# Kernel optimization log

Measured on AMD Instinct MI355X. Metric: run time of the kernel, lower is better.

## Reference

```python
import jax, jax.numpy as jnp
import numpy as np

B, S, D, H, DK = 2, 2048, 1024, 16, 64
NUM_BUCKETS, MAX_DIST = 32, 128
EPS = 1e-6


def _relative_position_bucket(rel, num_buckets=NUM_BUCKETS, max_distance=MAX_DIST):
    # bidirectional (T5 encoder) bucketing
    nb = num_buckets // 2
    bucket = (rel > 0).astype(jnp.int32) * nb
    n = jnp.abs(rel)
    max_exact = nb // 2
    is_small = n < max_exact
    large = max_exact + (
        jnp.log(jnp.maximum(n, 1).astype(jnp.float32) / max_exact)
        / np.log(max_distance / max_exact)
        * (nb - max_exact)
    ).astype(jnp.int32)
    large = jnp.minimum(large, nb - 1)
    return bucket + jnp.where(is_small, n, large)


def softmax1(logits):
    # off-by-one softmax: exp(x-m) / (sum(exp(x-m)) + exp(-m))
    m = jax.lax.stop_gradient(jnp.max(logits, axis=-1, keepdims=True))
    e = jnp.exp(logits - m)
    return e / (jnp.sum(e, axis=-1, keepdims=True) + jnp.exp(-m))


def setup_inputs() -> dict:
    key = jax.random.key(0)
    ks = jax.random.split(key, 8)
    scale = 0.02
    return {
        "hidden_states": jax.random.normal(ks[0], (B, S, D), dtype=jnp.float32),
        "delete_gate_mask": jax.random.normal(ks[1], (B, S, 1), dtype=jnp.float32),
        "ln_w": jnp.ones((D,), dtype=jnp.float32),
        "q_w": jax.random.normal(ks[2], (D, H * DK), dtype=jnp.float32) * scale,
        "k_w": jax.random.normal(ks[3], (D, H * DK), dtype=jnp.float32) * scale,
        "v_w": jax.random.normal(ks[4], (D, H * DK), dtype=jnp.float32) * scale,
        "o_w": jax.random.normal(ks[5], (H * DK, D), dtype=jnp.float32) * scale,
        "rel_emb": jax.random.normal(ks[6], (NUM_BUCKETS, H), dtype=jnp.float32) * scale,
    }


def reference(hidden_states, delete_gate_mask, ln_w, q_w, k_w, v_w, o_w, rel_emb):
    # T5LayerNorm (RMS norm, no mean subtraction, no bias)
    var = jnp.mean(jnp.square(hidden_states), axis=-1, keepdims=True)
    x = hidden_states * jax.lax.rsqrt(var + EPS) * ln_w

    # projections (T5 Linear layers have no bias, no 1/sqrt(d) scaling)
    q = (x @ q_w).reshape(B, S, H, DK).transpose(0, 2, 1, 3)  # bhqd
    k = (x @ k_w).reshape(B, S, H, DK).transpose(0, 2, 1, 3)  # bhkd
    v = (x @ v_w).reshape(B, S, H, DK).transpose(0, 2, 1, 3)  # bhkd

    scores = jnp.einsum("bhqd,bhkd->bhqk", q, k)

    # relative position bias: [1, H, S, S]
    pos = jnp.arange(S)
    rel = pos[None, :] - pos[:, None]  # key_pos - query_pos
    bucket = _relative_position_bucket(rel)  # [S, S]
    position_bias = rel_emb[bucket].transpose(2, 0, 1)[None]  # [1,H,S,S]

    # delete gate: [B,S,1] -> additive mask over key axis [B,1,1,S]
    gate = delete_gate_mask[..., 0][:, None, None, :]

    scores = scores + position_bias + gate
    attn = softmax1(scores.astype(jnp.float32)).astype(scores.dtype)

    attn_out = jnp.einsum("bhqk,bhkd->bhqd", attn, v)
    attn_out = attn_out.transpose(0, 2, 1, 3).reshape(B, S, H * DK) @ o_w

    # residual (dropout disabled at p=0)
    return hidden_states + attn_out
```

## Files before the change

### kernel.cpp

```cpp
#include <hip/hip_runtime.h>
#include <hip/hip_bf16.h>
#include <math.h>

typedef __attribute__((ext_vector_type(8))) short short8;
typedef __attribute__((ext_vector_type(4))) float f32x4;

#define S_LEN   2048
#define DMODEL  1024
#define NHEAD   16
#define HDK     64
#define NBATCH  2
#define MTOT    (NBATCH*S_LEN)
#define LOG2E   1.4426950408889634f

__device__ __forceinline__ unsigned short f2bf(float f) {
  union { float f; unsigned u; } c; c.f = f;
  unsigned r = c.u + 0x7FFFu + ((c.u >> 16) & 1u);
  return (unsigned short)(r >> 16);
}
__device__ __forceinline__ float bf2f(unsigned short u) {
  union { unsigned u; float f; } c; c.u = ((unsigned)u) << 16;
  return c.f;
}

__device__ __forceinline__ short8 lds_ld16(const unsigned short* p) {
  return *reinterpret_cast<const short8*>(p);
}

__device__ __forceinline__ void gload_lds16(const unsigned short* g, unsigned short* l) {
  __builtin_amdgcn_global_load_lds(
      (const __attribute__((address_space(1))) unsigned int*)g,
      (__attribute__((address_space(3))) unsigned int*)l, 16, 0, 0);
}

__global__ __launch_bounds__(256) void transpose_w_kernel(
    const float* __restrict__ qw, const float* __restrict__ kw,
    const float* __restrict__ vw, const float* __restrict__ ow,
    unsigned short* __restrict__ wqkv, unsigned short* __restrict__ wo) {
  int z = blockIdx.z;
  const float* src = (z==0)?qw:(z==1)?kw:(z==2)?vw:ow;
  unsigned short* dst = (z<3) ? (wqkv + (size_t)z*DMODEL*DMODEL) : wo;
  __shared__ float tile[32][33];
  int n0 = blockIdx.x*32, k0 = blockIdx.y*32;
  int tx = threadIdx.x, ty = threadIdx.y;
  for (int r = ty; r < 32; r += 8)
    tile[r][tx] = src[(size_t)(k0+r)*DMODEL + n0 + tx];
  __syncthreads();
  for (int r = ty; r < 32; r += 8)
    dst[(size_t)(n0+r)*DMODEL + k0 + tx] = f2bf(tile[tx][r]);
}

__global__ void bias_table_kernel(const float* __restrict__ rel_emb,
                                  float* __restrict__ btab) {
  int idx = blockIdx.x*256 + threadIdx.x;
  if (idx >= NHEAD*4095) return;
  int h = idx / 4095, rp = idx % 4095, rel = rp - 2047;
  int bucket = (rel > 0) ? 16 : 0;
  int n = (rel < 0) ? -rel : rel;
  int v;
  if (n < 8) v = n;
  else {
    float lrv = logf((float)n * 0.125f) / 2.7725887f * 8.0f;
    v = 8 + (int)lrv;
    if (v > 15) v = 15;
  }
  btab[idx] = rel_emb[(size_t)(bucket + v)*NHEAD + h] * LOG2E;
}

__global__ void eg_kernel(const float* __restrict__ gmask,
                          float* __restrict__ egf,
                          unsigned short* __restrict__ egb) {
  int i = blockIdx.x*256 + threadIdx.x;
  float e = __expf(gmask[i]);
  egf[i] = e;
  egb[i] = f2bf(e);
}

__global__ __launch_bounds__(256) void rmsnorm_kernel(
    const float* __restrict__ hs, const float* __restrict__ lnw,
    unsigned short* __restrict__ xo) {
  int row = blockIdx.x, t = threadIdx.x;
  const float4 v = ((const float4*)(hs + (size_t)row*DMODEL))[t];
  float ss = v.x*v.x + v.y*v.y + v.z*v.z + v.w*v.w;
  #pragma unroll
  for (int off = 32; off >= 1; off >>= 1) ss += __shfl_xor(ss, off, 64);
  __shared__ float wsum[4];
  if ((t & 63) == 0) wsum[t >> 6] = ss;
  __syncthreads();
  float tot = wsum[0] + wsum[1] + wsum[2] + wsum[3];
  float sc = rsqrtf(tot * (1.0f/DMODEL) + 1e-6f);
  const float4 lw = ((const float4*)lnw)[t];
  uint2 o;
  o.x = (unsigned)f2bf(v.x*sc*lw.x) | ((unsigned)f2bf(v.y*sc*lw.y) << 16);
  o.y = (unsigned)f2bf(v.z*sc*lw.z) | ((unsigned)f2bf(v.w*sc*lw.w) << 16);
  ((uint2*)(xo + (size_t)row*DMODEL))[t] = o;
}

template<int EPI>
__global__ __launch_bounds__(256) void gemm128(
    const unsigned short* __restrict__ X,
    const unsigned short* __restrict__ W,
    unsigned short* __restrict__ Oq, unsigned short* __restrict__ Ok,
    unsigned short* __restrict__ Ov,
    const float* __restrict__ resid, float* __restrict__ Of,
    const float* __restrict__ escale) {
  __shared__ unsigned short As[128*64];
  __shared__ unsigned short Bs[128*64];
  const int z = blockIdx.z;
  int m0, n0;
  const unsigned short *Ap, *Bp;
  if (EPI == 0 && z == 2) {
    m0 = blockIdx.y*128; n0 = blockIdx.x*128;
    Ap = W + (size_t)2*DMODEL*DMODEL; Bp = X;
  } else {
    m0 = blockIdx.x*128; n0 = blockIdx.y*128;
    Ap = X; Bp = W + ((EPI==0) ? (size_t)z*DMODEL*DMODEL : 0);
  }
  const int t = threadIdx.x, lane = t & 63, w = t >> 6;
  const int g = lane >> 4, lr = lane & 15;
  const int wr = (w >> 1)*64, wc = (w & 1)*64;

  f32x4 acc[4][4];
  #pragma unroll
  for (int mi = 0; mi < 4; mi++)
    #pragma unroll
    for (int ni = 0; ni < 4; ni++) acc[mi][ni] = (f32x4){0.f,0.f,0.f,0.f};

  const unsigned short* ag[4]; const unsigned short* bg[4];
  unsigned short* al[4]; unsigned short* bl[4];
  #pragma unroll
  for (int i = 0; i < 4; i++) {
    int slot = t + i*256, row = slot >> 3, c8 = slot & 7;
    int cs = c8 ^ (row & 7);
    ag[i] = Ap + (size_t)(m0 + row)*DMODEL + cs*8;
    bg[i] = Bp + (size_t)(n0 + row)*DMODEL + cs*8;
    al[i] = As + slot*8;
    bl[i] = Bs + slot*8;
  }

  for (int kk = 0; kk < DMODEL; kk += 64) {
    #pragma unroll
    for (int i = 0; i < 4; i++) {
      gload_lds16(ag[i] + kk, al[i]);
      gload_lds16(bg[i] + kk, bl[i]);
    }
    __syncthreads();
    #pragma unroll
    for (int ks = 0; ks < 2; ks++) {
      short8 af[4], bfr[4];
      #pragma unroll
      for (int mi = 0; mi < 4; mi++) {
        int R = wr + mi*16 + lr;
        af[mi] = lds_ld16(As + R*64 + (((ks*4 + g) ^ (R & 7)) << 3));
      }
      #pragma unroll
      for (int ni = 0; ni < 4; ni++) {
        int R = wc + ni*16 + lr;
        bfr[ni] = lds_ld16(Bs + R*64 + (((ks*4 + g) ^ (R & 7)) << 3));
      }
      #pragma unroll
      for (int mi = 0; mi < 4; mi++)
        #pragma unroll
        for (int ni = 0; ni < 4; ni++)
          acc[mi][ni] = __builtin_amdgcn_mfma_f32_16x16x32_bf16(af[mi], bfr[ni], acc[mi][ni], 0, 0, 0);
    }
    __syncthreads();
  }

  if (EPI == 0) {
    if (z < 2) {
      unsigned short* dst = (z == 0) ? Oq : Ok;
      const float osc = (z == 0) ? LOG2E : 1.0f;
      #pragma unroll
      for (int mi = 0; mi < 4; mi++) {
        #pragma unroll
        for (int r = 0; r < 4; r++) {
          int m = m0 + wr + mi*16 + g*4 + r;
          int b = m >> 11, s = m & (S_LEN-1);
          unsigned short* drow = dst + ((size_t)b*NHEAD*S_LEN + s)*HDK;
          #pragma unroll
          for (int ni = 0; ni < 4; ni++) {
            int n = n0 + wc + ni*16 + lr;
            int h = n >> 6, dcol = n & 63;
            drow[(size_t)h*S_LEN*HDK + dcol] = f2bf(acc[mi][ni][r] * osc);
          }
        }
      }
    } else {
      #pragma unroll
      for (int ni = 0; ni < 4; ni++) {
        int n = n0 + wc + ni*16 + lr;
        int b = n >> 11, s = n & (S_LEN-1);
        float e = escale[n];
        #pragma unroll
        for (int mi = 0; mi < 4; mi++)
          #pragma unroll
          for (int r = 0; r < 4; r++) {
            int m = m0 + wr + mi*16 + g*4 + r;
            Ov[((size_t)b*DMODEL + m)*S_LEN + s] = f2bf(acc[mi][ni][r] * e);
          }
      }
    }
  } else {
    #pragma unroll
    for (int mi = 0; mi < 4; mi++) {
      #pragma unroll
      for (int r = 0; r < 4; r++) {
        int m = m0 + wr + mi*16 + g*4 + r;
        const float* rrow = resid + (size_t)m*DMODEL;
        float* orow = Of + (size_t)m*DMODEL;
        #pragma unroll
        for (int ni = 0; ni < 4; ni++) {
          int n = n0 + wc + ni*16 + lr;
          orow[n] = rrow[n] + acc[mi][ni][r];
        }
      }
    }
  }
}

__global__ __launch_bounds__(256, 2) void combine_guard_dummy() {}
template<int SPLIT>
__global__ __launch_bounds__(256, 2) void attn_kernel(
    const unsigned short* __restrict__ Qg,
    const unsigned short* __restrict__ Kg,
    const unsigned short* __restrict__ Vtg,
    const float* __restrict__ btab,
    const unsigned short* __restrict__ egb,
    unsigned short* __restrict__ Og,
    unsigned short* __restrict__ Op0,
    unsigned short* __restrict__ Op1,
    float* __restrict__ lpart) {
  __shared__ __align__(16) unsigned short Kl[2][64][64];
  __shared__ __align__(16) unsigned short Vl[2][64][64];
  __shared__ __align__(16) unsigned short Pl[4][2][16*64];

  const int flat = blockIdx.x;
  const int xcd = flat & 7, j = flat >> 3;
  int bh, qx, half;
  if (SPLIT) { bh = xcd*4 + (j >> 5); int rest = j & 31; qx = rest >> 1; half = rest & 1; }
  else       { bh = xcd*4 + (j >> 4); qx = j & 15; half = 0; }
  const int b = bh >> 4, h = bh & 15;
  const int q0 = qx * 128;
  const int ktbase = SPLIT ? half*16 : 0;
  const int ktend  = SPLIT ? ktbase + 16 : 32;

  const int t = threadIdx.x, w = t >> 6, lane = t & 63;
  const int g = lane >> 4, lr = lane & 15, l7 = lane & 7;

  const unsigned short* Qb = Qg  + (size_t)bh*S_LEN*HDK;
  const unsigned short* Kb = Kg  + (size_t)bh*S_LEN*HDK;
  const unsigned short* Vb = Vtg + (size_t)bh*HDK*S_LEN;
  const unsigned short* ge = egb + (size_t)b*S_LEN;

  const int srow = t >> 3, sg0 = t & 7;
  const int cs = sg0 ^ (srow & 7);
  const unsigned short* kS0 = Kb + (size_t)srow*HDK + cs*8;
  const unsigned short* kS1 = Kb + (size_t)(srow+32)*HDK + cs*8;
  const unsigned short* vS0 = Vb + (size_t)srow*S_LEN + cs*8;
  const unsigned short* vS1 = Vb + (size_t)(srow+32)*S_LEN + cs*8;

#define STAGE(nb_, key_) do {                                          \
    gload_lds16(kS0 + (size_t)(key_)*HDK, &Kl[nb_][0][0] + t*8);       \
    gload_lds16(kS1 + (size_t)(key_)*HDK, &Kl[nb_][0][0] + t*8 + 2048);\
    gload_lds16(vS0 + (key_),             &Vl[nb_][0][0] + t*8);       \
    gload_lds16(vS1 + (key_),             &Vl[nb_][0][0] + t*8 + 2048);\
  } while (0)

  const int qs0A = q0 + w*32, qs0B = qs0A + 16;
  short8 qfA0 = *reinterpret_cast<const short8*>(Qb + (size_t)(qs0A+lr)*HDK + g*8);
  short8 qfA1 = *reinterpret_cast<const short8*>(Qb + (size_t)(qs0A+lr)*HDK + 32 + g*8);
  short8 qfB0 = *reinterpret_cast<const short8*>(Qb + (size_t)(qs0B+lr)*HDK + g*8);
  short8 qfB1 = *reinterpret_cast<const short8*>(Qb + (size_t)(qs0B+lr)*HDK + 32 + g*8);

  f32x4 accA[4], accB[4], l4A, l4B;
  #pragma unroll
  for (int n = 0; n < 4; n++) { accA[n] = (f32x4){0.f,0.f,0.f,0.f}; accB[n] = (f32x4){0.f,0.f,0.f,0.f}; }
  l4A = (f32x4){0.f,0.f,0.f,0.f}; l4B = (f32x4){0.f,0.f,0.f,0.f};

  const float* btb = btab + (size_t)h*4095 + 2047;
  const float cpos = btb[91];
  const float cneg = btb[-91];

  char* prowA = (char*)&Pl[w][0][0] + lr*128;
  char* prowB = (char*)&Pl[w][1][0] + lr*128;

  STAGE(0, ktbase*64);
  int cur = 0;
  for (int kt = ktbase; kt < ktend; ++kt) {
    const int key0 = kt*64;
    __syncthreads();

    if (kt + 1 < ktend) STAGE(cur^1, key0+64);

    short8 gv[2];
    #pragma unroll
    for (int c = 0; c < 2; c++) {
      short8 z8 = (short8){0,0,0,0,0,0,0,0};
      if (lr == 0)
        z8 = *reinterpret_cast<const short8*>(ge + key0 + c*32 + g*8);
      gv[c] = z8;
    }

    const int dbA = key0 - qs0A, dbB = key0 - qs0B;
    const bool bandA = (dbA > -154 && dbA < 106);
    const bool bandB = (dbB > -154 && dbB < 106);
    const float ccA = bandA ? 0.f : ((dbA > 0) ? cpos : cneg);
    const float ccB = bandB ? 0.f : ((dbB > 0) ? cpos : cneg);
    f32x4 svA[4], svB[4];
    {
      f32x4 zA = (f32x4){ccA,ccA,ccA,ccA}, zB = (f32x4){ccB,ccB,ccB,ccB};
      short8 bk[4];
      #pragma unroll
      for (int n = 0; n < 4; n++)
        bk[n] = lds_ld16(&Kl[cur][n*16 + lr][(g ^ l7) << 3]);
      __builtin_amdgcn_s_setprio(1);
      #pragma unroll
      for (int n = 0; n < 4; n++) {
        svA[n] = __builtin_amdgcn_mfma_f32_16x16x32_bf16(bk[n], qfA0, zA, 0, 0, 0);
        svB[n] = __builtin_amdgcn_mfma_f32_16x16x32_bf16(bk[n], qfB0, zB, 0, 0, 0);
      }
      __builtin_amdgcn_s_setprio(0);
      #pragma unroll
      for (int n = 0; n < 4; n++)
        bk[n] = lds_ld16(&Kl[cur][n*16 + lr][((4 + g) ^ l7) << 3]);
      __builtin_amdgcn_s_setprio(1);
      #pragma unroll
      for (int n = 0; n < 4; n++) {
        svA[n] = __builtin_amdgcn_mfma_f32_16x16x32_bf16(bk[n], qfA1, svA[n], 0, 0, 0);
        svB[n] = __builtin_amdgcn_mfma_f32_16x16x32_bf16(bk[n], qfB1, svB[n], 0, 0, 0);
      }
      __builtin_amdgcn_s_setprio(0);
    }

#define FINISH_SM(sv_, band_, db_, prow_)                                             \
    {                                                                                 \
      if (band_) {                                                                    \
        const float* btq = btb + ((db_) - lr);                                        \
        _Pragma("unroll") for (int n = 0; n < 4; n++)                                 \
          _Pragma("unroll") for (int r = 0; r < 4; r++)                               \
            sv_[n][r] += btq[n*16 + g*4 + r];                                         \
      }                                                                               \
      _Pragma("unroll") for (int n = 0; n < 4; n++)                                   \
        _Pragma("unroll") for (int r = 0; r < 4; r++)                                 \
          sv_[n][r] = exp2f(sv_[n][r]);                                               \
      _Pragma("unroll") for (int n = 0; n < 4; n++) {                                 \
        unsigned plo_, phi_;                                                          \
        asm("v_cvt_pk_bf16_f32 %0, %1, %2" : "=v"(plo_) : "v"(sv_[n][0]), "v"(sv_[n][1])); \
        asm("v_cvt_pk_bf16_f32 %0, %1, %2" : "=v"(phi_) : "v"(sv_[n][2]), "v"(sv_[n][3])); \
        uint2 pw_; pw_.x = plo_; pw_.y = phi_;                                        \
        *reinterpret_cast<uint2*>((prow_) + ((((2*n + (g>>1)) ^ l7) << 4) + ((g & 1) << 3))) = pw_; \
      }                                                                               \
    }
    FINISH_SM(svA, bandA, dbA, prowA)
    FINISH_SM(svB, bandB, dbB, prowB)
#undef FINISH_SM

    #pragma unroll
    for (int c = 0; c < 2; c++) {
      short8 bvf[4];
      #pragma unroll
      for (int n = 0; n < 4; n++)
        bvf[n] = lds_ld16(&Vl[cur][n*16 + lr][((4*c + g) ^ l7) << 3]);
      short8 paA = lds_ld16((const unsigned short*)(prowA + (((4*c + g) ^ l7) << 4)));
      short8 paB = lds_ld16((const unsigned short*)(prowB + (((4*c + g) ^ l7) << 4)));
      __builtin_amdgcn_s_setprio(1);
      #pragma unroll
      for (int n = 0; n < 4; n++) {
        accA[n] = __builtin_amdgcn_mfma_f32_16x16x32_bf16(paA, bvf[n], accA[n], 0, 0, 0);
        accB[n] = __builtin_amdgcn_mfma_f32_16x16x32_bf16(paB, bvf[n], accB[n], 0, 0, 0);
      }
      l4A = __builtin_amdgcn_mfma_f32_16x16x32_bf16(paA, gv[c], l4A, 0, 0, 0);
      l4B = __builtin_amdgcn_mfma_f32_16x16x32_bf16(paB, gv[c], l4B, 0, 0, 0);
      __builtin_amdgcn_s_setprio(0);
    }

    cur ^= 1;
  }

#define FINAL_SET(acc_, l4_, qs0_, op_)                                               \
  {                                                                                   \
    if (SPLIT) {                                                                      \
      if (lr == 0) {                                                                  \
        _Pragma("unroll") for (int r = 0; r < 4; r++)                                 \
          lpart[(size_t)half*(32*S_LEN) + (size_t)bh*S_LEN + (qs0_) + g*4 + r] = l4_[r]; \
      }                                                                               \
      _Pragma("unroll") for (int r = 0; r < 4; r++) {                                 \
        int srw = (qs0_) + g*4 + r;                                                   \
        unsigned short* orow = (op_) + ((size_t)bh*S_LEN + srw)*HDK;                  \
        _Pragma("unroll") for (int n = 0; n < 4; n++)                                 \
          orow[n*16 + lr] = f2bf(acc_[n][r]);                                         \
      }                                                                               \
    } else {                                                                          \
      _Pragma("unroll") for (int r = 0; r < 4; r++) {                                 \
        float lq = __shfl(l4_[r], g*16);                                              \
        float inv = 1.0f / (lq + 1.0f);                                               \
        int srw = (qs0_) + g*4 + r;                                                   \
        unsigned short* orow = Og + ((size_t)b*S_LEN + srw)*DMODEL + h*HDK;           \
        _Pragma("unroll") for (int n = 0; n < 4; n++)                                 \
          orow[n*16 + lr] = f2bf(acc_[n][r] * inv);                                   \
      }                                                                               \
    }                                                                                 \
  }
  unsigned short* op = half ? Op1 : Op0;
  FINAL_SET(accA, l4A, qs0A, op)
  FINAL_SET(accB, l4B, qs0B, op)
#undef FINAL_SET
#undef STAGE
}

__global__ __launch_bounds__(256) void combine_kernel(
    const unsigned short* __restrict__ Op0,
    const unsigned short* __restrict__ Op1,
    const float* __restrict__ lpart,
    unsigned short* __restrict__ ao) {
  int idx = blockIdx.x*256 + threadIdx.x;
  int row = idx >> 3;
  int d0 = (idx & 7) * 8;
  float l = lpart[row] + lpart[(size_t)32*S_LEN + row] + 1.0f;
  float inv = 1.0f / l;
  size_t src = (size_t)row*HDK + d0;
  short8 o0 = *reinterpret_cast<const short8*>(Op0 + src);
  short8 o1 = *reinterpret_cast<const short8*>(Op1 + src);
  int bh = row >> 11, s = row & (S_LEN-1), b = bh >> 4, h = bh & 15;
  unsigned short out[8];
  #pragma unroll
  for (int k = 0; k < 8; k++)
    out[k] = f2bf((bf2f((unsigned short)o0[k]) + bf2f((unsigned short)o1[k])) * inv);
  *reinterpret_cast<uint4*>(ao + ((size_t)(b*S_LEN + s))*DMODEL + h*HDK + d0) =
      *reinterpret_cast<const uint4*>(out);
}

extern "C" void kernel_launch(void* const* d_in, const int* in_sizes, int n_in,
                              void* d_out, int out_size, void* d_ws, size_t ws_size,
                              hipStream_t stream) {
  const float* hs   = (const float*)d_in[0];
  const float* gate = (const float*)d_in[1];
  const float* lnw  = (const float*)d_in[2];
  const float* qw   = (const float*)d_in[3];
  const float* kw   = (const float*)d_in[4];
  const float* vw   = (const float*)d_in[5];
  const float* ow   = (const float*)d_in[6];
  const float* rel  = (const float*)d_in[7];
  float* out = (float*)d_out;

  char* ws = (char*)d_ws;
  const size_t MB = 1ull << 20;
  unsigned short* xbf  = (unsigned short*)(ws);
  unsigned short* wqkv = (unsigned short*)(ws + 8*MB);
  unsigned short* wo   = (unsigned short*)(ws + 14*MB);
  unsigned short* qb   = (unsigned short*)(ws + 16*MB);
  unsigned short* kb   = (unsigned short*)(ws + 24*MB);
  unsigned short* vt   = (unsigned short*)(ws + 32*MB);
  unsigned short* ao   = (unsigned short*)(ws + 40*MB);
  float*          btab = (float*)(ws + 48*MB);
  float*          lpart= (float*)(ws + 48*MB + 256*1024);
  float*          egf  = (float*)(ws + 48*MB + 768*1024);
  unsigned short* egb  = (unsigned short*)(ws + 48*MB + 784*1024);
  unsigned short* op1  = (unsigned short*)(ws + 49*MB);
  unsigned short* op0  = xbf;
  const bool do_split = ws_size >= (57*MB);

  transpose_w_kernel<<<dim3(32,32,4), dim3(32,8), 0, stream>>>(qw, kw, vw, ow, wqkv, wo);
  bias_table_kernel<<<dim3(256), dim3(256), 0, stream>>>(rel, btab);
  eg_kernel<<<dim3(16), dim3(256), 0, stream>>>(gate, egf, egb);
  rmsnorm_kernel<<<dim3(MTOT), dim3(256), 0, stream>>>(hs, lnw, xbf);
  gemm128<0><<<dim3(MTOT/128, DMODEL/128, 3), dim3(256), 0, stream>>>(
      xbf, wqkv, qb, kb, vt, nullptr, nullptr, egf);
  if (do_split) {
    attn_kernel<1><<<dim3(1024), dim3(256), 0, stream>>>(
        qb, kb, vt, btab, egb, nullptr, op0, op1, lpart);
    combine_kernel<<<dim3(2048), dim3(256), 0, stream>>>(op0, op1, lpart, ao);
  } else {
    attn_kernel<0><<<dim3(512), dim3(256), 0, stream>>>(
        qb, kb, vt, btab, egb, ao, nullptr, nullptr, nullptr);
  }
  gemm128<1><<<dim3(MTOT/128, DMODEL/128, 1), dim3(256), 0, stream>>>(
      ao, wo, nullptr, nullptr, nullptr, hs, out, nullptr);
}
```

Measured before the change: 142.7 us.

## Drop split-K attention with combine; use 128-key tiles per barrier

Removes the two-way key-split attention path and its combine kernel, so each block processes all 2048 keys for its 128 queries with 512 blocks. K/V staging tiles grow from 64 to 128 keys, processed as two 64-key halves per barrier, which halves the number of synchronizations and deepens prefetch. This eliminates the partial-output write/read and an extra launch, at the cost of fewer blocks (less parallelism on many CUs) and doubled LDS use, which may reduce occupancy.

```diff
diff --git a/kernel.cpp b/kernel.cpp
--- a/kernel.cpp
+++ b/kernel.cpp
@@ -17,10 +17,6 @@
   union { float f; unsigned u; } c; c.f = f;
   unsigned r = c.u + 0x7FFFu + ((c.u >> 16) & 1u);
   return (unsigned short)(r >> 16);
-}
-__device__ __forceinline__ float bf2f(unsigned short u) {
-  union { unsigned u; float f; } c; c.u = ((unsigned)u) << 16;
-  return c.f;
 }
 
 __device__ __forceinline__ short8 lds_ld16(const unsigned short* p) {
@@ -219,31 +215,22 @@
   }
 }
 
-__global__ __launch_bounds__(256, 2) void combine_guard_dummy() {}
-template<int SPLIT>
 __global__ __launch_bounds__(256, 2) void attn_kernel(
     const unsigned short* __restrict__ Qg,
     const unsigned short* __restrict__ Kg,
     const unsigned short* __restrict__ Vtg,
     const float* __restrict__ btab,
     const unsigned short* __restrict__ egb,
-    unsigned short* __restrict__ Og,
-    unsigned short* __restrict__ Op0,
-    unsigned short* __restrict__ Op1,
-    float* __restrict__ lpart) {
-  __shared__ __align__(16) unsigned short Kl[2][64][64];
-  __shared__ __align__(16) unsigned short Vl[2][64][64];
+    unsigned short* __restrict__ Og) {
+  __shared__ __align__(16) unsigned short Kl[2][128*64];
+  __shared__ __align__(16) unsigned short Vl[2][64*128];
   __shared__ __align__(16) unsigned short Pl[4][2][16*64];
 
   const int flat = blockIdx.x;
   const int xcd = flat & 7, j = flat >> 3;
-  int bh, qx, half;
-  if (SPLIT) { bh = xcd*4 + (j >> 5); int rest = j & 31; qx = rest >> 1; half = rest & 1; }
-  else       { bh = xcd*4 + (j >> 4); qx = j & 15; half = 0; }
+  const int bh = xcd*4 + (j >> 4), qx = j & 15;
   const int b = bh >> 4, h = bh & 15;
   const int q0 = qx * 128;
-  const int ktbase = SPLIT ? half*16 : 0;
-  const int ktend  = SPLIT ? ktbase + 16 : 32;
 
   const int t = threadIdx.x, w = t >> 6, lane = t & 63;
   const int g = lane >> 4, lr = lane & 15, l7 = lane & 7;
@@ -253,19 +240,21 @@
   const unsigned short* Vb = Vtg + (size_t)bh*HDK*S_LEN;
   const unsigned short* ge = egb + (size_t)b*S_LEN;
 
-  const int srow = t >> 3, sg0 = t & 7;
-  const int cs = sg0 ^ (srow & 7);
-  const unsigned short* kS0 = Kb + (size_t)srow*HDK + cs*8;
-  const unsigned short* kS1 = Kb + (size_t)(srow+32)*HDK + cs*8;
-  const unsigned short* vS0 = Vb + (size_t)srow*S_LEN + cs*8;
-  const unsigned short* vS1 = Vb + (size_t)(srow+32)*S_LEN + cs*8;
-
+  const unsigned short* kS[4]; const unsigned short* vS[4]; int so[4];
+  #pragma unroll
+  for (int i = 0; i < 4; i++) {
+    int slot = t + i*256; so[i] = slot*8;
+    int krow = slot >> 3, kg = slot & 7;
+    kS[i] = Kb + (size_t)krow*HDK + ((kg ^ (krow & 7)) << 3);
+    int vrow = slot >> 4, vg = slot & 15;
+    int vcs = (vg & 8) | ((vg & 7) ^ (vrow & 7));
+    vS[i] = Vb + (size_t)vrow*S_LEN + vcs*8;
+  }
 #define STAGE(nb_, key_) do {                                          \
-    gload_lds16(kS0 + (size_t)(key_)*HDK, &Kl[nb_][0][0] + t*8);       \
-    gload_lds16(kS1 + (size_t)(key_)*HDK, &Kl[nb_][0][0] + t*8 + 2048);\
-    gload_lds16(vS0 + (key_),             &Vl[nb_][0][0] + t*8);       \
-    gload_lds16(vS1 + (key_),             &Vl[nb_][0][0] + t*8 + 2048);\
-  } while (0)
+    _Pragma("unroll") for (int i = 0; i < 4; i++) {                    \
+      gload_lds16(kS[i] + (size_t)(key_)*HDK, &Kl[nb_][0] + so[i]);    \
+      gload_lds16(vS[i] + (key_),             &Vl[nb_][0] + so[i]);    \
+    } } while (0)
 
   const int qs0A = q0 + w*32, qs0B = qs0A + 16;
   short8 qfA0 = *reinterpret_cast<const short8*>(Qb + (size_t)(qs0A+lr)*HDK + g*8);
@@ -285,150 +274,122 @@
   char* prowA = (char*)&Pl[w][0][0] + lr*128;
   char* prowB = (char*)&Pl[w][1][0] + lr*128;
 
-  STAGE(0, ktbase*64);
+  STAGE(0, 0);
   int cur = 0;
-  for (int kt = ktbase; kt < ktend; ++kt) {
-    const int key0 = kt*64;
+  for (int kt = 0; kt < S_LEN/128; ++kt) {
+    const int key0 = kt*128;
     __syncthreads();
 
-    if (kt + 1 < ktend) STAGE(cur^1, key0+64);
-
-    short8 gv[2];
+    if (kt + 1 < S_LEN/128) STAGE(cur^1, key0+128);
+
     #pragma unroll
-    for (int c = 0; c < 2; c++) {
-      short8 z8 = (short8){0,0,0,0,0,0,0,0};
-      if (lr == 0)
-        z8 = *reinterpret_cast<const short8*>(ge + key0 + c*32 + g*8);
-      gv[c] = z8;
-    }
-
-    const int dbA = key0 - qs0A, dbB = key0 - qs0B;
-    const bool bandA = (dbA > -154 && dbA < 106);
-    const bool bandB = (dbB > -154 && dbB < 106);
-    const float ccA = bandA ? 0.f : ((dbA > 0) ? cpos : cneg);
-    const float ccB = bandB ? 0.f : ((dbB > 0) ? cpos : cneg);
-    f32x4 svA[4], svB[4];
-    {
-      f32x4 zA = (f32x4){ccA,ccA,ccA,ccA}, zB = (f32x4){ccB,ccB,ccB,ccB};
-      short8 bk[4];
-      #pragma unroll
-      for (int n = 0; n < 4; n++)
-        bk[n] = lds_ld16(&Kl[cur][n*16 + lr][(g ^ l7) << 3]);
-      __builtin_amdgcn_s_setprio(1);
-      #pragma unroll
-      for (int n = 0; n < 4; n++) {
-        svA[n] = __builtin_amdgcn_mfma_f32_16x16x32_bf16(bk[n], qfA0, zA, 0, 0, 0);
-        svB[n] = __builtin_amdgcn_mfma_f32_16x16x32_bf16(bk[n], qfB0, zB, 0, 0, 0);
-      }
-      __builtin_amdgcn_s_setprio(0);
-      #pragma unroll
-      for (int n = 0; n < 4; n++)
-        bk[n] = lds_ld16(&Kl[cur][n*16 + lr][((4 + g) ^ l7) << 3]);
-      __builtin_amdgcn_s_setprio(1);
-      #pragma unroll
-      for (int n = 0; n < 4; n++) {
-        svA[n] = __builtin_amdgcn_mfma_f32_16x16x32_bf16(bk[n], qfA1, svA[n], 0, 0, 0);
-        svB[n] = __builtin_amdgcn_mfma_f32_16x16x32_bf16(bk[n], qfB1, svB[n], 0, 0, 0);
-      }
-      __builtin_amdgcn_s_setprio(0);
-    }
+    for (int hh = 0; hh < 2; hh++) {
+      const int k64 = key0 + hh*64;
+      const unsigned short* Klh = &Kl[cur][0] + hh*64*64;
+
+      short8 gvh[2];
+      #pragma unroll
+      for (int c = 0; c < 2; c++) {
+        short8 z8 = (short8){0,0,0,0,0,0,0,0};
+        if (lr == 0)
+          z8 = *reinterpret_cast<const short8*>(ge + k64 + c*32 + g*8);
+        gvh[c] = z8;
+      }
+
+      const int dbA = k64 - qs0A, dbB = k64 - qs0B;
+      const bool bandA = (dbA > -154 && dbA < 106);
+      const bool bandB = (dbB > -154 && dbB < 106);
+      const float ccA = bandA ? 0.f : ((dbA > 0) ? cpos : cneg);
+      const float ccB = bandB ? 0.f : ((dbB > 0) ? cpos : cneg);
+      f32x4 svA[4], svB[4];
+      {
+        f32x4 zA = (f32x4){ccA,ccA,ccA,ccA}, zB = (f32x4){ccB,ccB,ccB,ccB};
+        short8 bk[4];
+        #pragma unroll
+        for (int n = 0; n < 4; n++)
+          bk[n] = lds_ld16(Klh + (n*16 + lr)*64 + ((g ^ l7) << 3));
+        __builtin_amdgcn_s_setprio(1);
+        #pragma unroll
+        for (int n = 0; n < 4; n++) {
+          svA[n] = __builtin_amdgcn_mfma_f32_16x16x32_bf16(bk[n], qfA0, zA, 0, 0, 0);
+          svB[n] = __builtin_amdgcn_mfma_f32_16x16x32_bf16(bk[n], qfB0, zB, 0, 0, 0);
+        }
+        __builtin_amdgcn_s_setprio(0);
+        #pragma unroll
+        for (int n = 0; n < 4; n++)
+          bk[n] = lds_ld16(Klh + (n*16 + lr)*64 + (((4 + g) ^ l7) << 3));
+        __builtin_amdgcn_s_setprio(1);
+        #pragma unroll
+        for (int n = 0; n < 4; n++) {
+          svA[n] = __builtin_amdgcn_mfma_f32_16x16x32_bf16(bk[n], qfA1, svA[n], 0, 0, 0);
+          svB[n] = __builtin_amdgcn_mfma_f32_16x16x32_bf16(bk[n], qfB1, svB[n], 0, 0, 0);
+        }
+        __builtin_amdgcn_s_setprio(0);
+      }
 
 #define FINISH_SM(sv_, band_, db_, prow_)                                             \
-    {                                                                                 \
-      if (band_) {                                                                    \
-        const float* btq = btb + ((db_) - lr);                                        \
+      {                                                                               \
+        if (band_) {                                                                  \
+          const float* btq = btb + ((db_) - lr);                                      \
+          _Pragma("unroll") for (int n = 0; n < 4; n++)                               \
+            _Pragma("unroll") for (int r = 0; r < 4; r++)                             \
+              sv_[n][r] += btq[n*16 + g*4 + r];                                       \
+        }                                                                             \
         _Pragma("unroll") for (int n = 0; n < 4; n++)                                 \
           _Pragma("unroll") for (int r = 0; r < 4; r++)                               \
-            sv_[n][r] += btq[n*16 + g*4 + r];                                         \
-      }                                                                               \
+            sv_[n][r] = exp2f(sv_[n][r]);                                             \
+        _Pragma("unroll") for (int n = 0; n < 4; n++) {                               \
+          unsigned plo_, phi_;                                                        \
+          asm("v_cvt_pk_bf16_f32 %0, %1, %2" : "=v"(plo_) : "v"(sv_[n][0]), "v"(sv_[n][1])); \
+          asm("v_cvt_pk_bf16_f32 %0, %1, %2" : "=v"(phi_) : "v"(sv_[n][2]), "v"(sv_[n][3])); \
+          uint2 pw_; pw_.x = plo_; pw_.y = phi_;                                      \
+          *reinterpret_cast<uint2*>((prow_) + ((((2*n + (g>>1)) ^ l7) << 4) + ((g & 1) << 3))) = pw_; \
+        }                                                                             \
+      }
+      FINISH_SM(svA, bandA, dbA, prowA)
+      FINISH_SM(svB, bandB, dbB, prowB)
+#undef FINISH_SM
+
+      #pragma unroll
+      for (int c = 0; c < 2; c++) {
+        int gr = hh*8 + c*4 + g;
+        int grs = (gr & 8) | ((gr & 7) ^ l7);
+        short8 bvf[4];
+        #pragma unroll
+        for (int n = 0; n < 4; n++)
+          bvf[n] = lds_ld16(&Vl[cur][0] + (n*16 + lr)*128 + grs*8);
+        short8 paA = lds_ld16((const unsigned short*)(prowA + (((4*c + g) ^ l7) << 4)));
+        short8 paB = lds_ld16((const unsigned short*)(prowB + (((4*c + g) ^ l7) << 4)));
+        __builtin_amdgcn_s_setprio(1);
+        #pragma unroll
+        for (int n = 0; n < 4; n++) {
+          accA[n] = __builtin_amdgcn_mfma_f32_16x16x32_bf16(paA, bvf[n], accA[n], 0, 0, 0);
+          accB[n] = __builtin_amdgcn_mfma_f32_16x16x32_bf16(paB, bvf[n], accB[n], 0, 0, 0);
+        }
+        l4A = __builtin_amdgcn_mfma_f32_16x16x32_bf16(paA, gvh[c], l4A, 0, 0, 0);
+        l4B = __builtin_amdgcn_mfma_f32_16x16x32_bf16(paB, gvh[c], l4B, 0, 0, 0);
+        __builtin_amdgcn_s_setprio(0);
+      }
+    }
+
+    cur ^= 1;
+  }
+
+#define FINAL_SET(acc_, l4_, qs0_)                                                    \
+  {                                                                                   \
+    _Pragma("unroll") for (int r = 0; r < 4; r++) {                                   \
+      float lq = __shfl(l4_[r], g*16);                                                \
+      float inv = 1.0f / (lq + 1.0f);                                                 \
+      int srw = (qs0_) + g*4 + r;                                                     \
+      unsigned short* orow = Og + ((size_t)b*S_LEN + srw)*DMODEL + h*HDK;             \
       _Pragma("unroll") for (int n = 0; n < 4; n++)                                   \
-        _Pragma("unroll") for (int r = 0; r < 4; r++)                                 \
-          sv_[n][r] = exp2f(sv_[n][r]);                                               \
-      _Pragma("unroll") for (int n = 0; n < 4; n++) {                                 \
-        unsigned plo_, phi_;                                                          \
-        asm("v_cvt_pk_bf16_f32 %0, %1, %2" : "=v"(plo_) : "v"(sv_[n][0]), "v"(sv_[n][1])); \
-        asm("v_cvt_pk_bf16_f32 %0, %1, %2" : "=v"(phi_) : "v"(sv_[n][2]), "v"(sv_[n][3])); \
-        uint2 pw_; pw_.x = plo_; pw_.y = phi_;                                        \
-        *reinterpret_cast<uint2*>((prow_) + ((((2*n + (g>>1)) ^ l7) << 4) + ((g & 1) << 3))) = pw_; \
-      }                                                                               \
-    }
-    FINISH_SM(svA, bandA, dbA, prowA)
-    FINISH_SM(svB, bandB, dbB, prowB)
-#undef FINISH_SM
-
-    #pragma unroll
-    for (int c = 0; c < 2; c++) {
-      short8 bvf[4];
-      #pragma unroll
-      for (int n = 0; n < 4; n++)
-        bvf[n] = lds_ld16(&Vl[cur][n*16 + lr][((4*c + g) ^ l7) << 3]);
-      short8 paA = lds_ld16((const unsigned short*)(prowA + (((4*c + g) ^ l7) << 4)));
-      short8 paB = lds_ld16((const unsigned short*)(prowB + (((4*c + g) ^ l7) << 4)));
-      __builtin_amdgcn_s_setprio(1);
-      #pragma unroll
-      for (int n = 0; n < 4; n++) {
-        accA[n] = __builtin_amdgcn_mfma_f32_16x16x32_bf16(paA, bvf[n], accA[n], 0, 0, 0);
-        accB[n] = __builtin_amdgcn_mfma_f32_16x16x32_bf16(paB, bvf[n], accB[n], 0, 0, 0);
-      }
-      l4A = __builtin_amdgcn_mfma_f32_16x16x32_bf16(paA, gv[c], l4A, 0, 0, 0);
-      l4B = __builtin_amdgcn_mfma_f32_16x16x32_bf16(paB, gv[c], l4B, 0, 0, 0);
-      __builtin_amdgcn_s_setprio(0);
-    }
-
-    cur ^= 1;
-  }
-
-#define FINAL_SET(acc_, l4_, qs0_, op_)                                               \
-  {                                                                                   \
-    if (SPLIT) {                                                                      \
-      if (lr == 0) {                                                                  \
-        _Pragma("unroll") for (int r = 0; r < 4; r++)                                 \
-          lpart[(size_t)half*(32*S_LEN) + (size_t)bh*S_LEN + (qs0_) + g*4 + r] = l4_[r]; \
-      }                                                                               \
-      _Pragma("unroll") for (int r = 0; r < 4; r++) {                                 \
-        int srw = (qs0_) + g*4 + r;                                                   \
-        unsigned short* orow = (op_) + ((size_t)bh*S_LEN + srw)*HDK;                  \
-        _Pragma("unroll") for (int n = 0; n < 4; n++)                                 \
-          orow[n*16 + lr] = f2bf(acc_[n][r]);                                         \
-      }                                                                               \
-    } else {                                                                          \
-      _Pragma("unroll") for (int r = 0; r < 4; r++) {                                 \
-        float lq = __shfl(l4_[r], g*16);                                              \
-        float inv = 1.0f / (lq + 1.0f);                                               \
-        int srw = (qs0_) + g*4 + r;                                                   \
-        unsigned short* orow = Og + ((size_t)b*S_LEN + srw)*DMODEL + h*HDK;           \
-        _Pragma("unroll") for (int n = 0; n < 4; n++)                                 \
-          orow[n*16 + lr] = f2bf(acc_[n][r] * inv);                                   \
-      }                                                                               \
+        orow[n*16 + lr] = f2bf(acc_[n][r] * inv);                                     \
     }                                                                                 \
   }
-  unsigned short* op = half ? Op1 : Op0;
-  FINAL_SET(accA, l4A, qs0A, op)
-  FINAL_SET(accB, l4B, qs0B, op)
+  FINAL_SET(accA, l4A, qs0A)
+  FINAL_SET(accB, l4B, qs0B)
 #undef FINAL_SET
 #undef STAGE
-}
-
-__global__ __launch_bounds__(256) void combine_kernel(
-    const unsigned short* __restrict__ Op0,
-    const unsigned short* __restrict__ Op1,
-    const float* __restrict__ lpart,
-    unsigned short* __restrict__ ao) {
-  int idx = blockIdx.x*256 + threadIdx.x;
-  int row = idx >> 3;
-  int d0 = (idx & 7) * 8;
-  float l = lpart[row] + lpart[(size_t)32*S_LEN + row] + 1.0f;
-  float inv = 1.0f / l;
-  size_t src = (size_t)row*HDK + d0;
-  short8 o0 = *reinterpret_cast<const short8*>(Op0 + src);
-  short8 o1 = *reinterpret_cast<const short8*>(Op1 + src);
-  int bh = row >> 11, s = row & (S_LEN-1), b = bh >> 4, h = bh & 15;
-  unsigned short out[8];
-  #pragma unroll
-  for (int k = 0; k < 8; k++)
-    out[k] = f2bf((bf2f((unsigned short)o0[k]) + bf2f((unsigned short)o1[k])) * inv);
-  *reinterpret_cast<uint4*>(ao + ((size_t)(b*S_LEN + s))*DMODEL + h*HDK + d0) =
-      *reinterpret_cast<const uint4*>(out);
 }
 
 extern "C" void kernel_launch(void* const* d_in, const int* in_sizes, int n_in,
@@ -454,12 +415,8 @@
   unsigned short* vt   = (unsigned short*)(ws + 32*MB);
   unsigned short* ao   = (unsigned short*)(ws + 40*MB);
   float*          btab = (float*)(ws + 48*MB);
-  float*          lpart= (float*)(ws + 48*MB + 256*1024);
-  float*          egf  = (float*)(ws + 48*MB + 768*1024);
-  unsigned short* egb  = (unsigned short*)(ws + 48*MB + 784*1024);
-  unsigned short* op1  = (unsigned short*)(ws + 49*MB);
-  unsigned short* op0  = xbf;
-  const bool do_split = ws_size >= (57*MB);
+  float*          egf  = (float*)(ws + 48*MB + 256*1024);
+  unsigned short* egb  = (unsigned short*)(ws + 48*MB + 272*1024);
 
   transpose_w_kernel<<<dim3(32,32,4), dim3(32,8), 0, stream>>>(qw, kw, vw, ow, wqkv, wo);
   bias_table_kernel<<<dim3(256), dim3(256), 0, stream>>>(rel, btab);
@@ -467,14 +424,8 @@
   rmsnorm_kernel<<<dim3(MTOT), dim3(256), 0, stream>>>(hs, lnw, xbf);
   gemm128<0><<<dim3(MTOT/128, DMODEL/128, 3), dim3(256), 0, stream>>>(
       xbf, wqkv, qb, kb, vt, nullptr, nullptr, egf);
-  if (do_split) {
-    attn_kernel<1><<<dim3(1024), dim3(256), 0, stream>>>(
-        qb, kb, vt, btab, egb, nullptr, op0, op1, lpart);
-    combine_kernel<<<dim3(2048), dim3(256), 0, stream>>>(op0, op1, lpart, ao);
-  } else {
-    attn_kernel<0><<<dim3(512), dim3(256), 0, stream>>>(
-        qb, kb, vt, btab, egb, ao, nullptr, nullptr, nullptr);
-  }
+  attn_kernel<<<dim3(512), dim3(256), 0, stream>>>(
+      qb, kb, vt, btab, egb, ao);
   gemm128<1><<<dim3(MTOT/128, DMODEL/128, 1), dim3(256), 0, stream>>>(
       ao, wo, nullptr, nullptr, nullptr, hs, out, nullptr);
 }
```

Measured after the change: 140.3 us. Within noise of the previous version (-1.7%).
